# Kernel optimization log

Measured on AMD Instinct MI355X. Metric: run time of the kernel, lower is better.

## Reference

```python
import jax, jax.numpy as jnp
import numpy as np

TOPK = 10
NUM_CLASSES = 80
ALPHA = 0.5
BETA = 6.0
EPS = 1e-9
IOU_EPS = 1e-7


def _make_anchors(img=640, strides=(8, 16, 32)):
    pts = []
    for s in strides:
        n = img // s
        ax = (np.arange(n, dtype=np.float32) + 0.5) * s
        gy, gx = np.meshgrid(ax, ax, indexing='ij')
        pts.append(np.stack([gx.ravel(), gy.ravel()], axis=-1))
    return jnp.asarray(np.concatenate(pts, axis=0), dtype=jnp.float32)  # [8400, 2]


def setup_inputs() -> dict:
    key = jax.random.key(0)
    ks = jax.random.split(key, 8)
    bs, ng, nc = 32, 64, NUM_CLASSES
    anc_points = _make_anchors()
    na = anc_points.shape[0]  # 8400
    pd_scores = jax.random.uniform(ks[0], (bs, na, nc), dtype=jnp.float32)
    pwh = jax.random.uniform(ks[1], (bs, na, 2), minval=10.0, maxval=100.0)
    pxy = anc_points[None] + jax.random.normal(ks[2], (bs, na, 2)) * 8.0
    pd_bboxes = jnp.concatenate([pxy - pwh / 2, pxy + pwh / 2], axis=-1)
    gxy = jax.random.uniform(ks[3], (bs, ng, 2), minval=50.0, maxval=590.0)
    gwh = jax.random.uniform(ks[4], (bs, ng, 2), minval=20.0, maxval=200.0)
    gt_bboxes = jnp.clip(jnp.concatenate([gxy - gwh / 2, gxy + gwh / 2], axis=-1), 0.0, 640.0)
    gt_labels = jax.random.randint(ks[5], (bs, ng, 1), 0, nc)
    num_gt = jax.random.randint(ks[6], (bs,), 1, ng + 1)
    mask_gt = (jnp.arange(ng)[None, :] < num_gt[:, None])[..., None]  # bool [bs, ng, 1]
    return {"pd_scores": pd_scores, "pd_bboxes": pd_bboxes, "anc_points": anc_points,
            "gt_labels": gt_labels, "gt_bboxes": gt_bboxes, "mask_gt": mask_gt}


def _iou_xyxy(b1, b2):
    # b1: [bs, na, 1, 4], b2: [bs, 1, ng, 4] -> [bs, na, ng]
    inter_w = jnp.maximum(jnp.minimum(b1[..., 2], b2[..., 2]) - jnp.maximum(b1[..., 0], b2[..., 0]), 0.0)
    inter_h = jnp.maximum(jnp.minimum(b1[..., 3], b2[..., 3]) - jnp.maximum(b1[..., 1], b2[..., 1]), 0.0)
    inter = inter_w * inter_h
    a1 = (b1[..., 2] - b1[..., 0]) * (b1[..., 3] - b1[..., 1])
    a2 = (b2[..., 2] - b2[..., 0]) * (b2[..., 3] - b2[..., 1])
    return inter / (a1 + a2 - inter + IOU_EPS)


def _assign(pd_scores, pd_bboxes, anc_points, gt_labels, gt_bboxes, mask_gt):
    bs, na, nc = pd_scores.shape
    ng = gt_bboxes.shape[1]
    dt = pd_scores.dtype

    # --- candidates whose center lies strictly inside the GT box ---
    lt = gt_bboxes[:, None, :, :2]          # [bs,1,ng,2]
    rb = gt_bboxes[:, None, :, 2:]
    xy = anc_points[None, :, None, :]       # [1,na,1,2]
    deltas = jnp.concatenate([xy - lt, rb - xy], axis=-1)  # [bs,na,ng,4]
    mask_in_gts = deltas.min(axis=-1) > EPS                 # [bs,na,ng]
    valid = mask_gt[..., 0].astype(bool)                    # [bs,ng]
    mask = mask_in_gts & valid[:, None, :]

    # --- alignment metric = score[label]^alpha * iou^beta, zeroed outside mask ---
    labels = gt_labels[..., 0].astype(jnp.int32)            # [bs,ng]
    idx = jnp.broadcast_to(labels[:, None, :], (bs, na, ng))
    gathered = jnp.take_along_axis(pd_scores, idx, axis=2)  # [bs,na,ng]
    bbox_scores = jnp.where(mask, gathered, 0.0)
    overlaps = jnp.where(mask, _iou_xyxy(pd_bboxes[:, :, None, :], gt_bboxes[:, None, :, :]), 0.0)
    safe_scores = jnp.where(mask, gathered, 1.0)  # avoids 0**0.5 grad issues; masked out below
    align_metric = jnp.where(mask, safe_scores ** ALPHA * overlaps ** BETA, 0.0)

    # --- top-k anchors per GT (over anchor dim) ---
    k = min(TOPK, na)
    _, topk_idx = jax.lax.top_k(jnp.swapaxes(align_metric, 1, 2), k)  # [bs,ng,k]
    bidx = jnp.arange(bs)[:, None, None]
    gidx = jnp.arange(ng)[None, :, None]
    in_topk = jnp.zeros((bs, ng, na), dtype=bool).at[bidx, gidx, topk_idx].set(True)
    in_topk = jnp.swapaxes(in_topk, 1, 2) & valid[:, None, :]  # [bs,na,ng]
    mask_pos = (in_topk & mask).astype(dt)

    # --- resolve anchors assigned to multiple GTs by highest IoU ---
    multi = mask_pos.sum(-1, keepdims=True) > 1
    is_max = jax.nn.one_hot(jnp.argmax(overlaps, axis=-1), ng, dtype=dt)
    mask_pos = jnp.where(multi, is_max, mask_pos)
    fg_mask = mask_pos.sum(-1) > 0                  # [bs,na] bool
    target_gt_idx = jnp.argmax(mask_pos, axis=-1)   # [bs,na]

    # --- gather targets ---
    flat_idx = target_gt_idx + jnp.arange(bs)[:, None] * ng
    target_labels = jnp.maximum(gt_labels[..., 0].reshape(-1)[flat_idx], 0)  # [bs,na]
    target_bboxes = gt_bboxes.reshape(-1, 4)[flat_idx]                       # [bs,na,4]
    one_hot = jax.nn.one_hot(target_labels, nc, dtype=dt) * fg_mask[..., None].astype(dt)

    fgf = fg_mask[..., None].astype(dt)
    norm_align = jnp.maximum((align_metric * fgf).max(-1, keepdims=True), EPS)
    norm_overlap = jnp.maximum((overlaps * fgf).max(-1, keepdims=True), EPS)
    t_scores = ((align_metric / norm_align) * (overlaps / norm_overlap) * fgf).max(-1)  # [bs,na]
    target_scores = one_hot * t_scores[..., None]
    return target_labels, target_bboxes, target_scores, fg_mask, target_gt_idx


def reference(pd_scores, pd_bboxes, anc_points, gt_labels, gt_bboxes, mask_gt):
    return _assign(pd_scores, pd_bboxes, anc_points, gt_labels, gt_bboxes, mask_gt)
```

## Files before the change

kernel.cpp:

```cpp
#include <hip/hip_runtime.h>
#include <math.h>

#define NC 80
#define TOPKK 10
#define EPSF 1e-9f
#define IOU_EPSF 1e-7f
#define NA 8400
#define NGMAX 64

typedef float f4nt __attribute__((ext_vector_type(4)));

__device__ __forceinline__ float iou_xyxy(float px0, float py0, float px1, float py1,
                                          float parea,
                                          float gx0, float gy0, float gx1, float gy1,
                                          float garea) {
    float iw = fmaxf(fminf(px1, gx1) - fmaxf(px0, gx0), 0.0f);
    float ih = fmaxf(fminf(py1, gy1) - fmaxf(py0, gy0), 0.0f);
    float inter = iw * ih;
    return inter / (parea + garea - inter + IOU_EPSF);
}

__device__ __forceinline__ float align_metric(float s, float ov) {
    float ov2 = ov * ov;
    return sqrtf(s) * (ov2 * ov2 * ov2);
}

#define TK_INSERT(vv, aa) do {                                              \
    float nv[TOPKK]; int ni[TOPKK];                                         \
    _Pragma("unroll")                                                       \
    for (int q = 0; q < TOPKK; ++q) {                                       \
        bool keep = (lv[q] >= (vv));                                        \
        bool atp  = (q == 0) ? !keep : (!keep && (lv[q - 1] >= (vv)));      \
        nv[q] = keep ? lv[q] : (atp ? (vv) : lv[q - 1]);                    \
        ni[q] = keep ? li[q] : (atp ? (aa) : li[q - 1]);                    \
    }                                                                       \
    _Pragma("unroll")                                                       \
    for (int q = 0; q < TOPKK; ++q) { lv[q] = nv[q]; li[q] = ni[q]; }       \
} while (0)

#define TK_PROCESS() do {                                                   \
    float parea_ = (pb_p.z - pb_p.x) * (pb_p.w - pb_p.y);                   \
    float ov_ = iou_xyxy(pb_p.x, pb_p.y, pb_p.z, pb_p.w, parea_,            \
                         gb.x, gb.y, gb.z, gb.w, garea);                    \
    float v_ = align_metric(sc_p, ov_);                                     \
    if (v_ > 0.0f && v_ > lv[TOPKK - 1]) TK_INSERT(v_, a_p);                \
} while (0)

__global__ __launch_bounds__(256) void topk_rect_kernel(
    const float* __restrict__ pd_scores, const float* __restrict__ pd_bboxes,
    const int* __restrict__ gt_labels, const float* __restrict__ gt_bboxes,
    const int* __restrict__ mask_gt,
    int* __restrict__ idx_out, int ng, int total_bg)
{
    int lin = blockIdx.x * 4 + (threadIdx.x >> 6);
    if (lin >= total_bg) return;
    int b = lin / ng;
    int g = lin - b * ng;
    int lane = threadIdx.x & 63;
    int* __restrict__ slot = idx_out + (long)lin * TOPKK;

    if (mask_gt[b * ng + g] == 0) {
        if (lane < TOPKK) slot[lane] = -1;
        return;
    }

    int lab = gt_labels[b * ng + g];
    float4 gb = ((const float4*)gt_bboxes)[b * ng + g];
    float garea = (gb.z - gb.x) * (gb.w - gb.y);
    const float* __restrict__ srow = pd_scores + ((long)b * NA) * NC + lab;
    const float4* __restrict__ pbb = (const float4*)(pd_bboxes + (long)b * NA * 4);

    const int ls[3] = {8, 16, 32};
    const int ln[3] = {80, 40, 20};
    const int lb[3] = {0, 6400, 8000};
    int jlo[3], ilo[3], rw[3], cnt[3];
    float inv_rw[3];
    int tot = 0;
#pragma unroll
    for (int l = 0; l < 3; ++l) {
        float s = (float)ls[l];
        int j0 = (int)floorf(gb.x / s - 0.5f) - 1; if (j0 < 0) j0 = 0;
        int j1 = (int)ceilf (gb.z / s - 0.5f) + 1; if (j1 > ln[l] - 1) j1 = ln[l] - 1;
        int i0 = (int)floorf(gb.y / s - 0.5f) - 1; if (i0 < 0) i0 = 0;
        int i1 = (int)ceilf (gb.w / s - 0.5f) + 1; if (i1 > ln[l] - 1) i1 = ln[l] - 1;
        int w = j1 - j0 + 1; if (w < 0) w = 0;
        int h = i1 - i0 + 1; if (h < 0) h = 0;
        jlo[l] = j0; ilo[l] = i0; rw[l] = w; cnt[l] = w * h; tot += cnt[l];
        inv_rw[l] = (w > 0) ? 1.0f / (float)w : 0.0f;
    }

    float lv[TOPKK]; int li[TOPKK];
#pragma unroll
    for (int j = 0; j < TOPKK; ++j) { lv[j] = -1.0f; li[j] = -1; }

    int a_p = 0; bool ok_p = false; float sc_p = 0.0f;
    float4 pb_p = make_float4(0.f, 0.f, 0.f, 0.f);
    for (int t = lane; t < tot; t += 64) {
        int l = 0, r = t;
        if (r >= cnt[0]) { r -= cnt[0]; l = 1; }
        if (l == 1 && r >= cnt[1]) { r -= cnt[1]; l = 2; }
        int i = (int)((float)r * inv_rw[l]);
        int j = r - i * rw[l];
        if (j < 0) { --i; j += rw[l]; }
        else if (j >= rw[l]) { ++i; j -= rw[l]; }
        int ii = ilo[l] + i, jj = jlo[l] + j;
        int a  = lb[l] + ii * ln[l] + jj;
        float s  = (float)ls[l];
        float ax = (jj + 0.5f) * s, ay = (ii + 0.5f) * s;
        float d0 = ax - gb.x, d1 = ay - gb.y, d2 = gb.z - ax, d3 = gb.w - ay;
        float dmin = fminf(fminf(d0, d1), fminf(d2, d3));
        bool ok = dmin > EPSF;
        float4 pb = pb_p; float sc = 0.0f;
        if (ok) {
            pb = pbb[a];
            sc = srow[(long)a * NC];
        }
        if (ok_p) TK_PROCESS();
        a_p = a; pb_p = pb; sc_p = sc; ok_p = ok;
    }
    if (ok_p) TK_PROCESS();

    int m = 0;
    for (int it = 0; it < TOPKK; ++it) {
        unsigned long long myk = (lv[0] > 0.0f)
            ? (((unsigned long long)__float_as_uint(lv[0]) << 32)
               | (unsigned)(~(unsigned)li[0]))
            : 0ull;
        unsigned long long k = myk;
#pragma unroll
        for (int off = 32; off > 0; off >>= 1) {
            unsigned long long o = __shfl_xor(k, off, 64);
            k = (o > k) ? o : k;
        }
        if (k == 0ull) break;
        if (myk == k) {
            slot[it] = li[0];
#pragma unroll
            for (int q = 0; q < TOPKK - 1; ++q) { lv[q] = lv[q + 1]; li[q] = li[q + 1]; }
            lv[TOPKK - 1] = -1.0f; li[TOPKK - 1] = -1;
        }
        m++;
    }

    if (m < TOPKK && lane == 0) {
        int p = m;
        for (int a = 0; p < TOPKK && a < NA; ++a) {
            int l  = (a < 6400) ? 0 : ((a < 8000) ? 1 : 2);
            int rr = a - lb[l];
            int ii = rr / ln[l];
            int jj = rr - ii * ln[l];
            float s  = (float)ls[l];
            float ax = (jj + 0.5f) * s, ay = (ii + 0.5f) * s;
            float d0 = ax - gb.x, d1 = ay - gb.y, d2 = gb.z - ax, d3 = gb.w - ay;
            float dmin = fminf(fminf(d0, d1), fminf(d2, d3));
            bool positive = false;
            if (dmin > EPSF) {
                float4 pb = pbb[a];
                float parea = (pb.z - pb.x) * (pb.w - pb.y);
                float ov = iou_xyxy(pb.x, pb.y, pb.z, pb.w, parea,
                                    gb.x, gb.y, gb.z, gb.w, garea);
                float sc = srow[(long)a * NC];
                positive = (align_metric(sc, ov) > 0.0f);
            }
            if (!positive) slot[p++] = a;
        }
    }
}

__global__ __launch_bounds__(256) void assign_scores_kernel(
    const float* __restrict__ pd_scores, const float* __restrict__ pd_bboxes,
    const float* __restrict__ anc, const int* __restrict__ gt_labels,
    const float* __restrict__ gt_bboxes, const int* __restrict__ mask_gt,
    const int* __restrict__ idx_in,
    float* __restrict__ out_labels, float* __restrict__ out_bboxes,
    float* __restrict__ out_scores, float* __restrict__ out_fg,
    float* __restrict__ out_tgt, int ng, int blocksPerB)
{
    __shared__ float4 sgt[NGMAX];
    __shared__ float  sarea[NGMAX];
    __shared__ int    slab[NGMAX];
    __shared__ int    sgi[NGMAX];
    __shared__ int    snf;
    __shared__ float4 sgt0;
    __shared__ int    slab0s;
    __shared__ unsigned long long smask[256];
    __shared__ int    plab[256];
    __shared__ float  pt[256];

    int b  = blockIdx.x / blocksPerB;
    int a0 = (blockIdx.x - b * blocksPerB) * 256;
    int a  = a0 + threadIdx.x;

    smask[threadIdx.x] = 0ull;

    const int Lb[3] = {0, 6400, 8000};
    const int Lc[3] = {6400, 1600, 400};
    const int Ln[3] = {80, 40, 20};
    const int Ls[3] = {8, 16, 32};
    float ymin = 1e30f, ymax = -1e30f;
    {
        int aend = a0 + 255; if (aend > NA - 1) aend = NA - 1;
#pragma unroll
        for (int l = 0; l < 3; ++l) {
            int as_ = a0   > Lb[l]             ? a0   : Lb[l];
            int ae_ = aend < Lb[l] + Lc[l] - 1 ? aend : Lb[l] + Lc[l] - 1;
            if (as_ <= ae_) {
                int r0 = (as_ - Lb[l]) / Ln[l];
                int r1 = (ae_ - Lb[l]) / Ln[l];
                float s = (float)Ls[l];
                ymin = fminf(ymin, (r0 + 0.5f) * s);
                ymax = fmaxf(ymax, (r1 + 0.5f) * s);
            }
        }
    }

    if (threadIdx.x < 64) {
        int g = threadIdx.x;
        bool ok = false;
        float4 gb = make_float4(0.f, 0.f, 0.f, 0.f);
        if (g < ng && mask_gt[b * ng + g] != 0) {
            gb = ((const float4*)gt_bboxes)[b * ng + g];
            ok = (gb.y < ymax) && (gb.w > ymin);
        }
        unsigned long long bal = __ballot(ok);
        int pos = __popcll(bal & ((1ull << g) - 1ull));
        if (ok) {
            sgt[pos]   = gb;
            sarea[pos] = (gb.z - gb.x) * (gb.w - gb.y);
            slab[pos]  = gt_labels[b * ng + g];
            sgi[pos]   = g;
        }
        if (g == 0) {
            snf    = __popcll(bal);
            sgt0   = ((const float4*)gt_bboxes)[b * ng];
            slab0s = gt_labels[b * ng];
        }
    }
    __syncthreads();

    {
        int nent = ng * TOPKK;
        const int* lst = idx_in + (long)b * nent;
        for (int i = threadIdx.x; i < nent; i += 256) {
            int aa = lst[i];
            unsigned off = (unsigned)(aa - a0);
            if (aa >= 0 && off < 256u) {
                atomicOr(&smask[off], 1ull << (i / TOPKK));
            }
        }
    }
    __syncthreads();

    bool alive = (a < NA);
    int labi0 = slab0s < 0 ? 0 : slab0s;
    int labi = labi0; float t = 0.0f;

    if (alive) {
        long ba = (long)b * NA + a;
        unsigned long long w = smask[threadIdx.x];
        if (w == 0ull) {
            __builtin_nontemporal_store((float)labi0, &out_labels[ba]);
            f4nt g0; g0.x = sgt0.x; g0.y = sgt0.y; g0.z = sgt0.z; g0.w = sgt0.w;
            __builtin_nontemporal_store(g0, &((f4nt*)out_bboxes)[ba]);
            __builtin_nontemporal_store(0.0f, &out_fg[ba]);
            __builtin_nontemporal_store(0.0f, &out_tgt[ba]);
        } else {
            float ax = anc[a * 2 + 0];
            float ay = anc[a * 2 + 1];
            float4 pb = ((const float4*)pd_bboxes)[ba];
            float parea = (pb.z - pb.x) * (pb.w - pb.y);
            const float* __restrict__ srow = pd_scores + ba * NC;

            int cnt = 0, pos_k = 0, best_k = 0;
            float best_ov = 0.0f;
            float m_align = 0.0f, m_ov = 0.0f, t_raw = 0.0f;
            int nf = snf;

            for (int k = 0; k < nf; ++k) {
                float4 gbk = sgt[k];
                float d0 = ax - gbk.x, d1 = ay - gbk.y;
                float d2 = gbk.z - ax, d3 = gbk.w - ay;
                float dmin = fminf(fminf(d0, d1), fminf(d2, d3));
                bool mask = (dmin > EPSF);
                float ov = 0.0f, al = 0.0f;
                if (mask) {
                    ov = iou_xyxy(pb.x, pb.y, pb.z, pb.w, parea,
                                  gbk.x, gbk.y, gbk.z, gbk.w, sarea[k]);
                    float sc = srow[slab[k]];
                    al = align_metric(sc, ov);
                }
                bool pos = mask && ((w >> sgi[k]) & 1ull);
                if (pos) { if (cnt == 0) pos_k = k; cnt++; }
                if (ov > best_ov) { best_ov = ov; best_k = k; }
                m_align = fmaxf(m_align, al);
                m_ov    = fmaxf(m_ov, ov);
                t_raw   = fmaxf(t_raw, al * ov);
            }

            if (cnt == 0) {
                __builtin_nontemporal_store((float)labi0, &out_labels[ba]);
                f4nt g0; g0.x = sgt0.x; g0.y = sgt0.y; g0.z = sgt0.z; g0.w = sgt0.w;
                __builtin_nontemporal_store(g0, &((f4nt*)out_bboxes)[ba]);
                __builtin_nontemporal_store(0.0f, &out_fg[ba]);
                __builtin_nontemporal_store(0.0f, &out_tgt[ba]);
            } else {
                int tk = (cnt > 1) ? best_k : pos_k;
                labi = slab[tk]; if (labi < 0) labi = 0;
                __builtin_nontemporal_store((float)labi, &out_labels[ba]);
                float4 tb = sgt[tk];
                f4nt tb4; tb4.x = tb.x; tb4.y = tb.y; tb4.z = tb.z; tb4.w = tb.w;
                __builtin_nontemporal_store(tb4, &((f4nt*)out_bboxes)[ba]);
                __builtin_nontemporal_store(1.0f, &out_fg[ba]);
                __builtin_nontemporal_store((float)sgi[tk], &out_tgt[ba]);
                float na_ = fmaxf(m_align, EPSF);
                float no_ = fmaxf(m_ov, EPSF);
                t = (t_raw / na_) / no_;
            }
        }
    }

    plab[threadIdx.x] = labi;
    pt[threadIdx.x]   = t;
    __syncthreads();

    int cnt_rows = NA - a0; if (cnt_rows > 256) cnt_rows = 256;
    int tot4 = cnt_rows * (NC / 4);
    f4nt* __restrict__ oslab = (f4nt*)(out_scores + ((long)b * NA + a0) * NC);
    for (int i = threadIdx.x; i < tot4; i += 256) {
        int al = i / (NC / 4);
        int cg = (i - al * (NC / 4)) * 4;
        int lab = plab[al];
        float tv = pt[al];
        f4nt o;
        o.x = (cg     == lab) ? tv : 0.0f;
        o.y = (cg + 1 == lab) ? tv : 0.0f;
        o.z = (cg + 2 == lab) ? tv : 0.0f;
        o.w = (cg + 3 == lab) ? tv : 0.0f;
        __builtin_nontemporal_store(o, &oslab[i]);
    }
}

extern "C" void kernel_launch(void* const* d_in, const int* in_sizes, int n_in,
                              void* d_out, int out_size, void* d_ws, size_t ws_size,
                              hipStream_t stream) {
    const float* pd_scores = (const float*)d_in[0];
    const float* pd_bboxes = (const float*)d_in[1];
    const float* anc       = (const float*)d_in[2];
    const int*   gt_labels = (const int*)d_in[3];
    const float* gt_bboxes = (const float*)d_in[4];
    const int*   mask_gt   = (const int*)d_in[5];

    int na = in_sizes[2] / 2;
    int bs = in_sizes[0] / (na * NC);
    int ng = in_sizes[3] / bs;

    long nBA = (long)bs * na;
    float* out        = (float*)d_out;
    float* out_labels = out;
    float* out_bboxes = out + nBA;
    float* out_scores = out + nBA * 5;
    float* out_fg     = out + nBA * 85;
    float* out_tgt    = out + nBA * 86;

    int* idx = (int*)d_ws;

    int total_bg = bs * ng;
    int nblk = (total_bg + 3) / 4;
    topk_rect_kernel<<<nblk, 256, 0, stream>>>(
        pd_scores, pd_bboxes, gt_labels, gt_bboxes, mask_gt, idx, ng, total_bg);

    int bpb = (na + 255) / 256;
    assign_scores_kernel<<<bs * bpb, 256, 0, stream>>>(
        pd_scores, pd_bboxes, anc, gt_labels, gt_bboxes, mask_gt, idx,
        out_labels, out_bboxes, out_scores, out_fg, out_tgt, ng, bpb);
}
```

Baseline: 193.3 us.

## Split top-k per GT across two waves with shared-memory merge; branchless IoU loop

The top-k kernel now assigns two wavefronts to each GT box, each scanning half the candidate anchors. Their per-wave top-10 keys are merged through shared memory using rank counting, which shortens the serial scan per GT. The fallback scan for non-positive anchors becomes a wave-parallel ballot over the first 64 anchors instead of a single-lane serial loop. The assign kernel's inner GT loop computes the score gather and IoU unconditionally and selects with the mask, adding unroll 4 to expose more memory-level parallelism at the cost of extra loads.

```diff
diff --git a/kernel.cpp b/kernel.cpp
--- a/kernel.cpp
+++ b/kernel.cpp
@@ -52,117 +52,150 @@
     const int* __restrict__ mask_gt,
     int* __restrict__ idx_out, int ng, int total_bg)
 {
-    int lin = blockIdx.x * 4 + (threadIdx.x >> 6);
-    if (lin >= total_bg) return;
-    int b = lin / ng;
-    int g = lin - b * ng;
+    __shared__ unsigned long long skeys[2][2][TOPKK];
+
+    int pair = threadIdx.x >> 7;
+    int wv   = (threadIdx.x >> 6) & 1;
     int lane = threadIdx.x & 63;
-    int* __restrict__ slot = idx_out + (long)lin * TOPKK;
-
-    if (mask_gt[b * ng + g] == 0) {
-        if (lane < TOPKK) slot[lane] = -1;
-        return;
-    }
-
-    int lab = gt_labels[b * ng + g];
-    float4 gb = ((const float4*)gt_bboxes)[b * ng + g];
-    float garea = (gb.z - gb.x) * (gb.w - gb.y);
-    const float* __restrict__ srow = pd_scores + ((long)b * NA) * NC + lab;
-    const float4* __restrict__ pbb = (const float4*)(pd_bboxes + (long)b * NA * 4);
-
-    const int ls[3] = {8, 16, 32};
-    const int ln[3] = {80, 40, 20};
-    const int lb[3] = {0, 6400, 8000};
-    int jlo[3], ilo[3], rw[3], cnt[3];
-    float inv_rw[3];
-    int tot = 0;
-#pragma unroll
-    for (int l = 0; l < 3; ++l) {
-        float s = (float)ls[l];
-        int j0 = (int)floorf(gb.x / s - 0.5f) - 1; if (j0 < 0) j0 = 0;
-        int j1 = (int)ceilf (gb.z / s - 0.5f) + 1; if (j1 > ln[l] - 1) j1 = ln[l] - 1;
-        int i0 = (int)floorf(gb.y / s - 0.5f) - 1; if (i0 < 0) i0 = 0;
-        int i1 = (int)ceilf (gb.w / s - 0.5f) + 1; if (i1 > ln[l] - 1) i1 = ln[l] - 1;
-        int w = j1 - j0 + 1; if (w < 0) w = 0;
-        int h = i1 - i0 + 1; if (h < 0) h = 0;
-        jlo[l] = j0; ilo[l] = i0; rw[l] = w; cnt[l] = w * h; tot += cnt[l];
-        inv_rw[l] = (w > 0) ? 1.0f / (float)w : 0.0f;
-    }
-
-    float lv[TOPKK]; int li[TOPKK];
-#pragma unroll
-    for (int j = 0; j < TOPKK; ++j) { lv[j] = -1.0f; li[j] = -1; }
-
-    int a_p = 0; bool ok_p = false; float sc_p = 0.0f;
-    float4 pb_p = make_float4(0.f, 0.f, 0.f, 0.f);
-    for (int t = lane; t < tot; t += 64) {
-        int l = 0, r = t;
-        if (r >= cnt[0]) { r -= cnt[0]; l = 1; }
-        if (l == 1 && r >= cnt[1]) { r -= cnt[1]; l = 2; }
-        int i = (int)((float)r * inv_rw[l]);
-        int j = r - i * rw[l];
-        if (j < 0) { --i; j += rw[l]; }
-        else if (j >= rw[l]) { ++i; j -= rw[l]; }
-        int ii = ilo[l] + i, jj = jlo[l] + j;
-        int a  = lb[l] + ii * ln[l] + jj;
-        float s  = (float)ls[l];
-        float ax = (jj + 0.5f) * s, ay = (ii + 0.5f) * s;
-        float d0 = ax - gb.x, d1 = ay - gb.y, d2 = gb.z - ax, d3 = gb.w - ay;
-        float dmin = fminf(fminf(d0, d1), fminf(d2, d3));
-        bool ok = dmin > EPSF;
-        float4 pb = pb_p; float sc = 0.0f;
-        if (ok) {
-            pb = pbb[a];
-            sc = srow[(long)a * NC];
-        }
-        if (ok_p) TK_PROCESS();
-        a_p = a; pb_p = pb; sc_p = sc; ok_p = ok;
-    }
-    if (ok_p) TK_PROCESS();
-
-    int m = 0;
-    for (int it = 0; it < TOPKK; ++it) {
-        unsigned long long myk = (lv[0] > 0.0f)
-            ? (((unsigned long long)__float_as_uint(lv[0]) << 32)
-               | (unsigned)(~(unsigned)li[0]))
-            : 0ull;
-        unsigned long long k = myk;
-#pragma unroll
-        for (int off = 32; off > 0; off >>= 1) {
-            unsigned long long o = __shfl_xor(k, off, 64);
-            k = (o > k) ? o : k;
-        }
-        if (k == 0ull) break;
-        if (myk == k) {
-            slot[it] = li[0];
-#pragma unroll
-            for (int q = 0; q < TOPKK - 1; ++q) { lv[q] = lv[q + 1]; li[q] = li[q + 1]; }
-            lv[TOPKK - 1] = -1.0f; li[TOPKK - 1] = -1;
-        }
-        m++;
-    }
-
-    if (m < TOPKK && lane == 0) {
-        int p = m;
-        for (int a = 0; p < TOPKK && a < NA; ++a) {
-            int l  = (a < 6400) ? 0 : ((a < 8000) ? 1 : 2);
-            int rr = a - lb[l];
-            int ii = rr / ln[l];
-            int jj = rr - ii * ln[l];
+    int lin  = blockIdx.x * 2 + pair;
+    bool active = (lin < total_bg);
+
+    int b = 0, g = 0;
+    bool validgt = false;
+    int* __restrict__ slot = idx_out;
+    if (active) {
+        b = lin / ng;
+        g = lin - b * ng;
+        slot = idx_out + (long)lin * TOPKK;
+        validgt = (mask_gt[b * ng + g] != 0);
+        if (!validgt && wv == 0 && lane < TOPKK) slot[lane] = -1;
+    }
+
+    float4 gb = make_float4(0.f, 0.f, 0.f, 0.f);
+    float garea = 0.0f;
+    const float* __restrict__ srow = pd_scores;
+    const float4* __restrict__ pbb = (const float4*)pd_bboxes;
+
+    if (active && validgt) {
+        int lab = gt_labels[b * ng + g];
+        gb = ((const float4*)gt_bboxes)[b * ng + g];
+        garea = (gb.z - gb.x) * (gb.w - gb.y);
+        srow = pd_scores + ((long)b * NA) * NC + lab;
+        pbb  = (const float4*)(pd_bboxes + (long)b * NA * 4);
+
+        if (lane < TOPKK) skeys[pair][wv][lane] = 0ull;
+
+        const int ls[3] = {8, 16, 32};
+        const int ln[3] = {80, 40, 20};
+        const int lb[3] = {0, 6400, 8000};
+        int jlo[3], ilo[3], rw[3], cnt[3];
+        float inv_rw[3];
+        int tot = 0;
+#pragma unroll
+        for (int l = 0; l < 3; ++l) {
+            float s = (float)ls[l];
+            int j0 = (int)floorf(gb.x / s - 0.5f) - 1; if (j0 < 0) j0 = 0;
+            int j1 = (int)ceilf (gb.z / s - 0.5f) + 1; if (j1 > ln[l] - 1) j1 = ln[l] - 1;
+            int i0 = (int)floorf(gb.y / s - 0.5f) - 1; if (i0 < 0) i0 = 0;
+            int i1 = (int)ceilf (gb.w / s - 0.5f) + 1; if (i1 > ln[l] - 1) i1 = ln[l] - 1;
+            int w = j1 - j0 + 1; if (w < 0) w = 0;
+            int h = i1 - i0 + 1; if (h < 0) h = 0;
+            jlo[l] = j0; ilo[l] = i0; rw[l] = w; cnt[l] = w * h; tot += cnt[l];
+            inv_rw[l] = (w > 0) ? 1.0f / (float)w : 0.0f;
+        }
+
+        float lv[TOPKK]; int li[TOPKK];
+#pragma unroll
+        for (int j = 0; j < TOPKK; ++j) { lv[j] = -1.0f; li[j] = -1; }
+
+        int a_p = 0; bool ok_p = false; float sc_p = 0.0f;
+        float4 pb_p = make_float4(0.f, 0.f, 0.f, 0.f);
+        for (int t = (wv << 6) + lane; t < tot; t += 128) {
+            int l = 0, r = t;
+            if (r >= cnt[0]) { r -= cnt[0]; l = 1; }
+            if (l == 1 && r >= cnt[1]) { r -= cnt[1]; l = 2; }
+            int i = (int)((float)r * inv_rw[l]);
+            int j = r - i * rw[l];
+            if (j < 0) { --i; j += rw[l]; }
+            else if (j >= rw[l]) { ++i; j -= rw[l]; }
+            int ii = ilo[l] + i, jj = jlo[l] + j;
+            int a  = lb[l] + ii * ln[l] + jj;
             float s  = (float)ls[l];
             float ax = (jj + 0.5f) * s, ay = (ii + 0.5f) * s;
             float d0 = ax - gb.x, d1 = ay - gb.y, d2 = gb.z - ax, d3 = gb.w - ay;
             float dmin = fminf(fminf(d0, d1), fminf(d2, d3));
+            bool ok = dmin > EPSF;
+            float4 pb = pb_p; float sc = 0.0f;
+            if (ok) {
+                pb = pbb[a];
+                sc = srow[(long)a * NC];
+            }
+            if (ok_p) TK_PROCESS();
+            a_p = a; pb_p = pb; sc_p = sc; ok_p = ok;
+        }
+        if (ok_p) TK_PROCESS();
+
+        for (int it = 0; it < TOPKK; ++it) {
+            unsigned long long myk = (lv[0] > 0.0f)
+                ? (((unsigned long long)__float_as_uint(lv[0]) << 32)
+                   | (unsigned)(~(unsigned)li[0]))
+                : 0ull;
+            unsigned long long k = myk;
+#pragma unroll
+            for (int off = 32; off > 0; off >>= 1) {
+                unsigned long long o = __shfl_xor(k, off, 64);
+                k = (o > k) ? o : k;
+            }
+            if (k == 0ull) break;
+            if (lane == 0) skeys[pair][wv][it] = k;
+            if (myk == k) {
+#pragma unroll
+                for (int q = 0; q < TOPKK - 1; ++q) { lv[q] = lv[q + 1]; li[q] = li[q + 1]; }
+                lv[TOPKK - 1] = -1.0f; li[TOPKK - 1] = -1;
+            }
+        }
+    }
+
+    __syncthreads();
+
+    if (active && validgt && wv == 0) {
+        unsigned long long mykey = 0ull;
+        int posn = 0;
+        bool has = false;
+        if (lane < 2 * TOPKK) {
+            int side = (lane >= TOPKK) ? 1 : 0;
+            int si   = lane - side * TOPKK;
+            mykey = skeys[pair][side][si];
+            int cgt = 0;
+#pragma unroll
+            for (int j = 0; j < TOPKK; ++j) {
+                unsigned long long o = skeys[pair][side ^ 1][j];
+                cgt += (o > mykey) ? 1 : 0;
+            }
+            posn = si + cgt;
+            has = (mykey != 0ull) && (posn < TOPKK);
+            if (has) slot[posn] = (int)(~(unsigned)(mykey & 0xffffffffu));
+        }
+        unsigned long long bal = __ballot(has);
+        int m = __popcll(bal);
+
+        if (m < TOPKK) {
+            int a = lane;
+            float ax = (a + 0.5f) * 8.0f, ay = 4.0f;
+            float d0 = ax - gb.x, d1 = ay - gb.y, d2 = gb.z - ax, d3 = gb.w - ay;
+            float dmin = fminf(fminf(d0, d1), fminf(d2, d3));
             bool positive = false;
             if (dmin > EPSF) {
-                float4 pb = pbb[a];
-                float parea = (pb.z - pb.x) * (pb.w - pb.y);
-                float ov = iou_xyxy(pb.x, pb.y, pb.z, pb.w, parea,
-                                    gb.x, gb.y, gb.z, gb.w, garea);
-                float sc = srow[(long)a * NC];
-                positive = (align_metric(sc, ov) > 0.0f);
-            }
-            if (!positive) slot[p++] = a;
+                float4 pbv = pbb[a];
+                float parea = (pbv.z - pbv.x) * (pbv.w - pbv.y);
+                float ovf = iou_xyxy(pbv.x, pbv.y, pbv.z, pbv.w, parea,
+                                     gb.x, gb.y, gb.z, gb.w, garea);
+                float scf = srow[(long)a * NC];
+                positive = (align_metric(scf, ovf) > 0.0f);
+            }
+            unsigned long long zb = __ballot(!positive);
+            int rank = __popcll(zb & ((1ull << lane) - 1ull));
+            if (!positive && rank < TOPKK - m) slot[m + rank] = a;
         }
     }
 }
@@ -217,16 +250,16 @@
     if (threadIdx.x < 64) {
         int g = threadIdx.x;
         bool ok = false;
-        float4 gb = make_float4(0.f, 0.f, 0.f, 0.f);
+        float4 gbv = make_float4(0.f, 0.f, 0.f, 0.f);
         if (g < ng && mask_gt[b * ng + g] != 0) {
-            gb = ((const float4*)gt_bboxes)[b * ng + g];
-            ok = (gb.y < ymax) && (gb.w > ymin);
+            gbv = ((const float4*)gt_bboxes)[b * ng + g];
+            ok = (gbv.y < ymax) && (gbv.w > ymin);
         }
         unsigned long long bal = __ballot(ok);
         int pos = __popcll(bal & ((1ull << g) - 1ull));
         if (ok) {
-            sgt[pos]   = gb;
-            sarea[pos] = (gb.z - gb.x) * (gb.w - gb.y);
+            sgt[pos]   = gbv;
+            sarea[pos] = (gbv.z - gbv.x) * (gbv.w - gbv.y);
             slab[pos]  = gt_labels[b * ng + g];
             sgi[pos]   = g;
         }
@@ -276,19 +309,18 @@
             float m_align = 0.0f, m_ov = 0.0f, t_raw = 0.0f;
             int nf = snf;
 
+#pragma unroll 4
             for (int k = 0; k < nf; ++k) {
                 float4 gbk = sgt[k];
                 float d0 = ax - gbk.x, d1 = ay - gbk.y;
                 float d2 = gbk.z - ax, d3 = gbk.w - ay;
                 float dmin = fminf(fminf(d0, d1), fminf(d2, d3));
                 bool mask = (dmin > EPSF);
-                float ov = 0.0f, al = 0.0f;
-                if (mask) {
-                    ov = iou_xyxy(pb.x, pb.y, pb.z, pb.w, parea,
-                                  gbk.x, gbk.y, gbk.z, gbk.w, sarea[k]);
-                    float sc = srow[slab[k]];
-                    al = align_metric(sc, ov);
-                }
+                float sc = srow[slab[k]];
+                float iouv = iou_xyxy(pb.x, pb.y, pb.z, pb.w, parea,
+                                      gbk.x, gbk.y, gbk.z, gbk.w, sarea[k]);
+                float ov = mask ? iouv : 0.0f;
+                float al = align_metric(sc, ov);
                 bool pos = mask && ((w >> sgi[k]) & 1ull);
                 if (pos) { if (cnt == 0) pos_k = k; cnt++; }
                 if (ov > best_ov) { best_ov = ov; best_k = k; }
@@ -365,7 +397,7 @@
     int* idx = (int*)d_ws;
 
     int total_bg = bs * ng;
-    int nblk = (total_bg + 3) / 4;
+    int nblk = (total_bg + 1) / 2;
     topk_rect_kernel<<<nblk, 256, 0, stream>>>(
         pd_scores, pd_bboxes, gt_labels, gt_bboxes, mask_gt, idx, ng, total_bg);
 
```

New measurement: 194.0 us. Within noise of the previous version (+0.4%).
